# Kernel optimization log

Hardware: AMD Instinct MI355X
Metric: run time of the kernel (lower is better)

## Reference

```python
import jax, jax.numpy as jnp
import numpy as np

ALPHA = 0.2          # LeakyReLU negative slope
NEG_INF = -9e15      # masking value from the original module


def setup_inputs() -> dict:
    key = jax.random.key(0)
    kw, ka, k1, k2, k3 = jax.random.split(key, 5)
    B, N1, N2, F, O = 4, 2048, 2048, 256, 256
    word = jax.random.normal(kw, (B, N2, F), dtype=jnp.float32)
    # 0/1 hypergraph incidence matrix (float, as in the torch module)
    adj = jax.random.randint(ka, (B, N1, N2), 0, 2).astype(jnp.float32)
    stdv = 1.0 / np.sqrt(O)
    W1 = jax.random.uniform(k1, (F, O), jnp.float32, -stdv, stdv)
    W2 = jax.random.uniform(k2, (F, O), jnp.float32, -stdv, stdv)
    w3 = jax.random.uniform(k3, (2 * O, 1), jnp.float32, -stdv, stdv)
    return {"word": word, "adj": adj, "W1": W1, "W2": W2, "w3": w3}


def reference(word, adj, W1, W2, w3):
    # word: [B, N2, F]; adj: [B, N1, N2]; W1/W2: [F, O]; w3: [2O, 1]
    O = W1.shape[1]
    # mean-pool neighbor features per hyperedge (row-normalized adj)
    deg = jnp.sum(adj, axis=-1, keepdims=True)                 # [B, N1, 1]
    deg = jnp.where(deg > 0, deg, jnp.ones_like(deg))
    mp = jnp.matmul(adj / deg, word)                           # [B, N1, F]
    # The original builds 4D tensors h1[b,i,j,:] = adj[b,i,j]*word[b,j,:] and
    # h_mp[b,i,j,:] = adj[b,i,j]*mp[b,i,:], projects both and dots with w3.
    # Since scaling commutes with the linear maps, the scalar score is
    #   adj[b,i,j] * (word[b,j] @ W1 @ w3_a + mp[b,i] @ W2 @ w3_b)
    w3a = w3[:O, 0]                                            # pairs with w1h
    w3b = w3[O:, 0]                                            # pairs with w2h
    s1 = jnp.einsum('bnf,fo,o->bn', word, W1, w3a)             # [B, N2]
    s2 = jnp.einsum('bnf,fo,o->bn', mp, W2, w3b)               # [B, N1]
    pre = adj * (s2[:, :, None] + s1[:, None, :])              # [B, N1, N2]
    alpha = jnp.exp(jax.nn.leaky_relu(pre, ALPHA))
    attention = jnp.where(adj > 0, alpha, NEG_INF)
    attention_edge = jax.nn.softmax(attention, axis=2)         # over N2
    edge = jnp.matmul(attention_edge, word)                    # [B, N1, F]
    return edge
```

## Files before the change

kernel.cpp:

```cpp
#include <hip/hip_runtime.h>

#define B 4
#define N 2048
#define F 256
#define O 256
#define LOG2E 1.4426950408889634f
#define NEG_BIG -9000000000000000.0f

typedef _Float16 f16;
typedef f16 f16x8 __attribute__((ext_vector_type(8)));
typedef f16 f16x4 __attribute__((ext_vector_type(4)));
typedef float f32x16 __attribute__((ext_vector_type(16)));

#define WS_V1 0
#define WS_V2 256
#define WS_T1 512
#define WS_T2 (512 + B*N)
#define WS_S2 (512 + 2*B*N)
#define WS_CR (512 + 3*B*N)
#define WS_WN (512 + 4*B*N)
#define WT_OFF (1u << 20)
#define MK_OFF (6u << 20)

__device__ __forceinline__ float alpha_of(float pre2) {
  return __builtin_amdgcn_exp2f(fmaxf(pre2, 0.2f * pre2));
}

__global__ __launch_bounds__(256) void k_v(const float* __restrict__ W1,
                                           const float* __restrict__ W2,
                                           const float* __restrict__ w3,
                                           float* __restrict__ ws) {
  int tid = threadIdx.x;
  int lane = tid & 63;
  int f = blockIdx.x * 4 + (tid >> 6);
  float a = 0.f, b = 0.f;
  #pragma unroll
  for (int k = 0; k < 4; ++k) {
    int o = lane + 64 * k;
    a += W1[f * O + o] * w3[o];
    b += W2[f * O + o] * w3[O + o];
  }
  #pragma unroll
  for (int off = 32; off > 0; off >>= 1) {
    a += __shfl_down(a, off);
    b += __shfl_down(b, off);
  }
  if (lane == 0) {
    ws[WS_V1 + f] = a;
    ws[WS_V2 + f] = b;
  }
}

__global__ __launch_bounds__(256) void k_prep(const float* __restrict__ word,
                                              float* __restrict__ ws,
                                              f16* __restrict__ wordT) {
  __shared__ float v1s[F], v2s[F];
  __shared__ __align__(16) f16 tile[F][40];
  int t = threadIdx.x;
  int k0 = blockIdx.x * 32;
  int b = blockIdx.y;

  if (t < 64)       ((float4*)v1s)[t]      = ((const float4*)(ws + WS_V1))[t];
  else if (t < 128) ((float4*)v2s)[t - 64] = ((const float4*)(ws + WS_V2))[t - 64];
  __syncthreads();

  int r = t >> 3;
  int cg = t & 7;
  const float* wrow = word + ((size_t)(b * N + k0 + r)) * F;
  float a = 0.f, bb = 0.f;
  #pragma unroll
  for (int i = 0; i < 8; ++i) {
    int c = i * 32 + cg * 4;
    float4 w = *(const float4*)(wrow + c);
    float4 x1 = *(const float4*)(v1s + c);
    float4 x2 = *(const float4*)(v2s + c);
    a  += w.x * x1.x + w.y * x1.y + w.z * x1.z + w.w * x1.w;
    bb += w.x * x2.x + w.y * x2.y + w.z * x2.z + w.w * x2.w;
    tile[c + 0][r] = (f16)w.x;
    tile[c + 1][r] = (f16)w.y;
    tile[c + 2][r] = (f16)w.z;
    tile[c + 3][r] = (f16)w.w;
  }
  #pragma unroll
  for (int off = 4; off > 0; off >>= 1) {
    a  += __shfl_down(a, off);
    bb += __shfl_down(bb, off);
  }
  if (cg == 0) {
    ws[WS_T1 + b * N + k0 + r] = a * LOG2E;
    ws[WS_T2 + b * N + k0 + r] = bb;
  }
  __syncthreads();

  f16* dst = wordT + ((size_t)(b * F + t)) * N + k0;
  *(f16x8*)(dst + 0)  = *(const f16x8*)&tile[t][0];
  *(f16x8*)(dst + 8)  = *(const f16x8*)&tile[t][8];
  *(f16x8*)(dst + 16) = *(const f16x8*)&tile[t][16];
  *(f16x8*)(dst + 24) = *(const f16x8*)&tile[t][24];
}

__global__ __launch_bounds__(256) void k_stats(const float* __restrict__ adj,
                                               float* __restrict__ ws,
                                               unsigned char* __restrict__ mask) {
  int row = blockIdx.x;
  int b = row >> 11;
  int t = threadIdx.x;
  int wid = t >> 6, lane = t & 63;
  const float* arow = adj + (size_t)row * N;
  const float* t1b = ws + WS_T1 + b * N;
  const float* t2b = ws + WS_T2 + b * N;

  float4 a0 = *(const float4*)(arow + t * 8);
  float4 a1 = *(const float4*)(arow + t * 8 + 4);
  float4 u0 = *(const float4*)(t2b + t * 8);
  float4 u1 = *(const float4*)(t2b + t * 8 + 4);
  float deg = a0.x + a0.y + a0.z + a0.w + a1.x + a1.y + a1.z + a1.w;
  float dot = a0.x * u0.x + a0.y * u0.y + a0.z * u0.z + a0.w * u0.w +
              a1.x * u1.x + a1.y * u1.y + a1.z * u1.z + a1.w * u1.w;
  unsigned mb = (a0.x > 0.f ? 1u : 0u) | (a0.y > 0.f ? 2u : 0u) |
                (a0.z > 0.f ? 4u : 0u) | (a0.w > 0.f ? 8u : 0u) |
                (a1.x > 0.f ? 16u : 0u) | (a1.y > 0.f ? 32u : 0u) |
                (a1.z > 0.f ? 64u : 0u) | (a1.w > 0.f ? 128u : 0u);
  mask[(size_t)row * 256 + t] = (unsigned char)mb;

  #pragma unroll
  for (int off = 32; off > 0; off >>= 1) {
    deg += __shfl_down(deg, off);
    dot += __shfl_down(dot, off);
  }
  __shared__ float rd[4], rt[4], rm[4], rz[4];
  if (lane == 0) { rd[wid] = deg; rt[wid] = dot; }
  __syncthreads();
  deg = rd[0] + rd[1] + rd[2] + rd[3];
  dot = rt[0] + rt[1] + rt[2] + rt[3];
  float degc = deg > 0.f ? deg : 1.f;
  float s2p = (dot / degc) * LOG2E;

  float4 p0 = *(const float4*)(t1b + t * 8);
  float4 p1 = *(const float4*)(t1b + t * 8 + 4);
  float al[8];
  al[0] = (mb & 1)   ? alpha_of(p0.x + s2p) : NEG_BIG;
  al[1] = (mb & 2)   ? alpha_of(p0.y + s2p) : NEG_BIG;
  al[2] = (mb & 4)   ? alpha_of(p0.z + s2p) : NEG_BIG;
  al[3] = (mb & 8)   ? alpha_of(p0.w + s2p) : NEG_BIG;
  al[4] = (mb & 16)  ? alpha_of(p1.x + s2p) : NEG_BIG;
  al[5] = (mb & 32)  ? alpha_of(p1.y + s2p) : NEG_BIG;
  al[6] = (mb & 64)  ? alpha_of(p1.z + s2p) : NEG_BIG;
  al[7] = (mb & 128) ? alpha_of(p1.w + s2p) : NEG_BIG;
  float m = NEG_BIG;
  #pragma unroll
  for (int j = 0; j < 8; ++j) m = fmaxf(m, al[j]);
  #pragma unroll
  for (int off = 32; off > 0; off >>= 1) m = fmaxf(m, __shfl_down(m, off));
  if (lane == 0) rm[wid] = m;
  __syncthreads();
  m = fmaxf(fmaxf(rm[0], rm[1]), fmaxf(rm[2], rm[3]));

  float negmL = -m * LOG2E;
  float z = 0.f;
  #pragma unroll
  for (int j = 0; j < 8; ++j) z += __builtin_amdgcn_exp2f(fmaf(al[j], LOG2E, negmL));
  #pragma unroll
  for (int off = 32; off > 0; off >>= 1) z += __shfl_down(z, off);
  if (lane == 0) rz[wid] = z;
  __syncthreads();
  if (t == 0) {
    z = rz[0] + rz[1] + rz[2] + rz[3];
    ws[WS_S2 + row] = s2p;
    if (deg > 0.f) {
      ws[WS_CR + row] = negmL - log2f(z);
      ws[WS_WN + row] = 0.f;
    } else {
      ws[WS_CR + row] = 0.f;
      ws[WS_WN + row] = 1.0f / (float)N;
    }
  }
}

__global__ __launch_bounds__(512, 2) void k_gemm(const f16* __restrict__ wordT,
                                                 const unsigned char* __restrict__ maskg,
                                                 const float* __restrict__ ws,
                                                 float* __restrict__ out) {
  __shared__ __align__(16) f16 Aw[2][8][512];
  __shared__ __align__(16) float t1S[N];
  __shared__ __align__(16) unsigned maskS[32][64];
  __shared__ float sSC[96];

  const int t = threadIdx.x;
  const int row0 = blockIdx.x * 32;
  const int b = row0 >> 11;

  *(float4*)&t1S[t * 4] = *(const float4*)(ws + WS_T1 + b * N + t * 4);
  *(uint4*)&maskS[t >> 4][(t & 15) * 4] =
      *(const uint4*)(maskg + (size_t)(row0 + (t >> 4)) * 256 + (t & 15) * 16);
  if (t < 32) {
    sSC[t]      = ws[WS_S2 + row0 + t];
    sSC[32 + t] = ws[WS_CR + row0 + t];
    sSC[64 + t] = ws[WS_WN + row0 + t];
  }
  __syncthreads();

  const int gl = t & 63;
  const int gc = t >> 6;
  const int grow = gl & 31;
  const int gkb = gc * 16 + (gl >> 5) * 8;
  const float rs2 = sSC[grow], rcr = sSC[32 + grow], rwn = sSC[64 + grow];

  const int lw = t & 63;
  const int wv = t >> 6;
  const int fcol = wv * 32 + (lw & 31);
  const f16* bptr = wordT + ((size_t)(b * F + fcol)) * N + (lw >> 5) * 8;

  f32x16 acc = {0.f,0.f,0.f,0.f,0.f,0.f,0.f,0.f,0.f,0.f,0.f,0.f,0.f,0.f,0.f,0.f};

  #define GENW(IT, BUF)                                                        \
    {                                                                          \
      const int kg = (IT) * 128 + gkb;                                         \
      const unsigned mw = maskS[grow][kg >> 5] >> (kg & 31);                   \
      const float4 tv0 = *(const float4*)&t1S[kg];                             \
      const float4 tv1 = *(const float4*)&t1S[kg + 4];                         \
      const float tvv[8] = {tv0.x, tv0.y, tv0.z, tv0.w,                        \
                            tv1.x, tv1.y, tv1.z, tv1.w};                       \
      f16x8 h;                                                                 \
      _Pragma("unroll")                                                        \
      for (int j = 0; j < 8; ++j) {                                            \
        float p = tvv[j] + rs2;                                                \
        float al = __builtin_amdgcn_exp2f(fmaxf(p, 0.2f * p));                 \
        float wsel = __builtin_amdgcn_exp2f(fmaf(al, LOG2E, rcr));             \
        float w = ((mw >> j) & 1u) ? wsel : rwn;                               \
        h[j] = (f16)w;                                                         \
      }                                                                        \
      *(f16x8*)&Aw[BUF][gc][gl * 8] = h;                                       \
    }

  GENW(0, 0)
  __syncthreads();

  for (int it = 0; it < 16; ++it) {
    const int cur = it & 1;
    f16x8 bf[8];
    const f16* bp = bptr + it * 128;
    #pragma unroll
    for (int c = 0; c < 8; ++c) bf[c] = *(const f16x8*)(bp + c * 16);
    if (it < 15) GENW(it + 1, cur ^ 1)
    #pragma unroll
    for (int c = 0; c < 8; ++c) {
      const f16x8 af = *(const f16x8*)&Aw[cur][c][lw * 8];
      acc = __builtin_amdgcn_mfma_f32_32x32x16_f16(af, bf[c], acc, 0, 0, 0);
    }
    __syncthreads();
  }

  #pragma unroll
  for (int reg = 0; reg < 16; ++reg) {
    int lr = (reg & 3) + 8 * (reg >> 2) + 4 * (lw >> 5);
    out[(size_t)(row0 + lr) * F + fcol] = acc[reg];
  }
}

extern "C" void kernel_launch(void* const* d_in, const int* in_sizes, int n_in,
                              void* d_out, int out_size, void* d_ws, size_t ws_size,
                              hipStream_t stream) {
  const float* word = (const float*)d_in[0];
  const float* adj  = (const float*)d_in[1];
  const float* W1   = (const float*)d_in[2];
  const float* W2   = (const float*)d_in[3];
  const float* w3   = (const float*)d_in[4];
  float* out = (float*)d_out;
  float* ws  = (float*)d_ws;
  f16* wordT = (f16*)((char*)d_ws + WT_OFF);
  unsigned char* mask = (unsigned char*)d_ws + MK_OFF;

  k_v<<<64, 256, 0, stream>>>(W1, W2, w3, ws);
  k_prep<<<dim3(N / 32, B), 256, 0, stream>>>(word, ws, wordT);
  k_stats<<<B * N, 256, 0, stream>>>(adj, ws, mask);
  k_gemm<<<(B * N) / 32, 512, 0, stream>>>(wordT, mask, ws, out);
}
```

Before: 148.5 us.

## Retile attention GEMM to 64-row blocks split across feature halves with MFMA-swizzled wordT

```diff
diff --git a/kernel.cpp b/kernel.cpp
--- a/kernel.cpp
+++ b/kernel.cpp
@@ -9,7 +9,6 @@
 
 typedef _Float16 f16;
 typedef f16 f16x8 __attribute__((ext_vector_type(8)));
-typedef f16 f16x4 __attribute__((ext_vector_type(4)));
 typedef float f32x16 __attribute__((ext_vector_type(16)));
 
 #define WS_V1 0
@@ -92,11 +91,16 @@
   }
   __syncthreads();
 
-  f16* dst = wordT + ((size_t)(b * F + t)) * N + k0;
-  *(f16x8*)(dst + 0)  = *(const f16x8*)&tile[t][0];
-  *(f16x8*)(dst + 8)  = *(const f16x8*)&tile[t][8];
-  *(f16x8*)(dst + 16) = *(const f16x8*)&tile[t][16];
-  *(f16x8*)(dst + 24) = *(const f16x8*)&tile[t][24];
+  size_t base = (size_t)b * F * N;
+  #pragma unroll
+  for (int i = 0; i < 4; ++i) {
+    int idx = t + 256 * i;
+    int ft = idx >> 7, c = (idx >> 6) & 1, l = idx & 63;
+    int f = ft * 32 + (l & 31);
+    int rr = c * 16 + ((l >> 5) * 8);
+    f16x8 h = *(const f16x8*)&tile[f][rr];
+    *(f16x8*)(wordT + base + ((size_t)((ft * 128 + (k0 >> 4) + c) * 64 + l)) * 8) = h;
+  }
 }
 
 __global__ __launch_bounds__(256) void k_stats(const float* __restrict__ adj,
@@ -177,75 +181,92 @@
   }
 }
 
-__global__ __launch_bounds__(512, 2) void k_gemm(const f16* __restrict__ wordT,
+__global__ __launch_bounds__(512, 1) void k_gemm(const f16* __restrict__ wordT,
                                                  const unsigned char* __restrict__ maskg,
                                                  const float* __restrict__ ws,
                                                  float* __restrict__ out) {
-  __shared__ __align__(16) f16 Aw[2][8][512];
+  __shared__ __align__(16) f16 Aw[2][2][8][512];
   __shared__ __align__(16) float t1S[N];
-  __shared__ __align__(16) unsigned maskS[32][64];
-  __shared__ float sSC[96];
+  __shared__ float sSC[192];
 
   const int t = threadIdx.x;
-  const int row0 = blockIdx.x * 32;
+  const int rb = blockIdx.x >> 1, fh = blockIdx.x & 1;
+  const int row0 = rb * 64;
   const int b = row0 >> 11;
 
   *(float4*)&t1S[t * 4] = *(const float4*)(ws + WS_T1 + b * N + t * 4);
-  *(uint4*)&maskS[t >> 4][(t & 15) * 4] =
-      *(const uint4*)(maskg + (size_t)(row0 + (t >> 4)) * 256 + (t & 15) * 16);
-  if (t < 32) {
-    sSC[t]      = ws[WS_S2 + row0 + t];
-    sSC[32 + t] = ws[WS_CR + row0 + t];
-    sSC[64 + t] = ws[WS_WN + row0 + t];
+  if (t < 64) {
+    sSC[t]       = ws[WS_S2 + row0 + t];
+    sSC[64 + t]  = ws[WS_CR + row0 + t];
+    sSC[128 + t] = ws[WS_WN + row0 + t];
   }
   __syncthreads();
 
   const int gl = t & 63;
-  const int gc = t >> 6;
-  const int grow = gl & 31;
-  const int gkb = gc * 16 + (gl >> 5) * 8;
-  const float rs2 = sSC[grow], rcr = sSC[32 + grow], rwn = sSC[64 + grow];
+  const int gc = (t >> 6) & 3;
+  const int rh_g = t >> 8;
+  const int koff = (gl >> 5) * 8;
+  const int rowL = rh_g * 32 + (gl & 31);
+  const float rs2 = sSC[rowL], rcr = sSC[64 + rowL], rwn = sSC[128 + rowL];
+  const unsigned* mrow = (const unsigned*)(maskg + (size_t)(row0 + rowL) * 256);
 
   const int lw = t & 63;
   const int wv = t >> 6;
-  const int fcol = wv * 32 + (lw & 31);
-  const f16* bptr = wordT + ((size_t)(b * F + fcol)) * N + (lw >> 5) * 8;
+  const int rh = wv >> 2;
+  const int ftile = fh * 4 + (wv & 3);
+  const int fcol = ftile * 32 + (lw & 31);
+  const f16* wtb = wordT + (size_t)b * F * N;
 
   f32x16 acc = {0.f,0.f,0.f,0.f,0.f,0.f,0.f,0.f,0.f,0.f,0.f,0.f,0.f,0.f,0.f,0.f};
 
-  #define GENW(IT, BUF)                                                        \
+  #define GENW(IT, BUF, MW)                                                    \
     {                                                                          \
-      const int kg = (IT) * 128 + gkb;                                         \
-      const unsigned mw = maskS[grow][kg >> 5] >> (kg & 31);                   \
-      const float4 tv0 = *(const float4*)&t1S[kg];                             \
-      const float4 tv1 = *(const float4*)&t1S[kg + 4];                         \
-      const float tvv[8] = {tv0.x, tv0.y, tv0.z, tv0.w,                        \
-                            tv1.x, tv1.y, tv1.z, tv1.w};                       \
-      f16x8 h;                                                                 \
+      const int kb = (IT) * 128 + gc * 32 + koff;                              \
+      const float4 ta0 = *(const float4*)&t1S[kb];                             \
+      const float4 ta1 = *(const float4*)&t1S[kb + 4];                         \
+      const float4 tb0 = *(const float4*)&t1S[kb + 16];                        \
+      const float4 tb1 = *(const float4*)&t1S[kb + 20];                        \
+      const float ta[8] = {ta0.x, ta0.y, ta0.z, ta0.w, ta1.x, ta1.y, ta1.z, ta1.w}; \
+      const float tb[8] = {tb0.x, tb0.y, tb0.z, tb0.w, tb1.x, tb1.y, tb1.z, tb1.w}; \
+      const unsigned m0 = (MW) >> koff;                                        \
+      const unsigned m1 = (MW) >> (16 + koff);                                 \
+      f16x8 h0, h1;                                                            \
       _Pragma("unroll")                                                        \
       for (int j = 0; j < 8; ++j) {                                            \
-        float p = tvv[j] + rs2;                                                \
-        float al = __builtin_amdgcn_exp2f(fmaxf(p, 0.2f * p));                 \
-        float wsel = __builtin_amdgcn_exp2f(fmaf(al, LOG2E, rcr));             \
-        float w = ((mw >> j) & 1u) ? wsel : rwn;                               \
-        h[j] = (f16)w;                                                         \
+        float p0 = ta[j] + rs2;                                                \
+        float a0v = __builtin_amdgcn_exp2f(fmaxf(p0, 0.2f * p0));              \
+        float w0 = ((m0 >> j) & 1u) ? __builtin_amdgcn_exp2f(fmaf(a0v, LOG2E, rcr)) : rwn; \
+        h0[j] = (f16)w0;                                                       \
+        float p1 = tb[j] + rs2;                                                \
+        float a1v = __builtin_amdgcn_exp2f(fmaxf(p1, 0.2f * p1));              \
+        float w1 = ((m1 >> j) & 1u) ? __builtin_amdgcn_exp2f(fmaf(a1v, LOG2E, rcr)) : rwn; \
+        h1[j] = (f16)w1;                                                       \
       }                                                                        \
-      *(f16x8*)&Aw[BUF][gc][gl * 8] = h;                                       \
-    }
-
-  GENW(0, 0)
+      *(f16x8*)&Aw[BUF][rh_g][gc * 2][gl * 8]     = h0;                        \
+      *(f16x8*)&Aw[BUF][rh_g][gc * 2 + 1][gl * 8] = h1;                        \
+    }
+
+  {
+    unsigned mw0 = mrow[gc];
+    GENW(0, 0, mw0)
+  }
   __syncthreads();
 
   for (int it = 0; it < 16; ++it) {
     const int cur = it & 1;
+    const f16* bp = wtb + ((size_t)(ftile * 128 + it * 8) * 64 + lw) * 8;
     f16x8 bf[8];
-    const f16* bp = bptr + it * 128;
     #pragma unroll
-    for (int c = 0; c < 8; ++c) bf[c] = *(const f16x8*)(bp + c * 16);
-    if (it < 15) GENW(it + 1, cur ^ 1)
+    for (int c = 0; c < 8; ++c) bf[c] = *(const f16x8*)(bp + (size_t)c * 512);
+
+    if (it < 15) {
+      unsigned mwn = mrow[(it + 1) * 4 + gc];
+      GENW(it + 1, cur ^ 1, mwn)
+    }
+
     #pragma unroll
     for (int c = 0; c < 8; ++c) {
-      const f16x8 af = *(const f16x8*)&Aw[cur][c][lw * 8];
+      const f16x8 af = *(const f16x8*)&Aw[cur][rh][c][lw * 8];
       acc = __builtin_amdgcn_mfma_f32_32x32x16_f16(af, bf[c], acc, 0, 0, 0);
     }
     __syncthreads();
@@ -253,7 +274,7 @@
 
   #pragma unroll
   for (int reg = 0; reg < 16; ++reg) {
-    int lr = (reg & 3) + 8 * (reg >> 2) + 4 * (lw >> 5);
+    int lr = rh * 32 + (reg & 3) + 8 * (reg >> 2) + 4 * (lw >> 5);
     out[(size_t)(row0 + lr) * F + fcol] = acc[reg];
   }
 }
@@ -274,5 +295,5 @@
   k_v<<<64, 256, 0, stream>>>(W1, W2, w3, ws);
   k_prep<<<dim3(N / 32, B), 256, 0, stream>>>(word, ws, wordT);
   k_stats<<<B * N, 256, 0, stream>>>(adj, ws, mask);
-  k_gemm<<<(B * N) / 32, 512, 0, stream>>>(wordT, mask, ws, out);
-}
+  k_gemm<<<(B * N) / 64 * 2, 512, 0, stream>>>(wordT, mask, ws, out);
+}
```

Result: faster. 132.5 us (-10.8%).

## Materialize fp16 attention weights in stats kernel and swizzle word for direct-load GEMM

Applied to the files above, without the earlier changes.

```diff
diff --git a/kernel.cpp b/kernel.cpp
--- a/kernel.cpp
+++ b/kernel.cpp
@@ -9,18 +9,14 @@
 
 typedef _Float16 f16;
 typedef f16 f16x8 __attribute__((ext_vector_type(8)));
-typedef f16 f16x4 __attribute__((ext_vector_type(4)));
 typedef float f32x16 __attribute__((ext_vector_type(16)));
 
 #define WS_V1 0
 #define WS_V2 256
 #define WS_T1 512
 #define WS_T2 (512 + B*N)
-#define WS_S2 (512 + 2*B*N)
-#define WS_CR (512 + 3*B*N)
-#define WS_WN (512 + 4*B*N)
 #define WT_OFF (1u << 20)
-#define MK_OFF (6u << 20)
+#define W_OFF  (8u << 20)
 
 __device__ __forceinline__ float alpha_of(float pre2) {
   return __builtin_amdgcn_exp2f(fmaxf(pre2, 0.2f * pre2));
@@ -92,16 +88,21 @@
   }
   __syncthreads();
 
-  f16* dst = wordT + ((size_t)(b * F + t)) * N + k0;
-  *(f16x8*)(dst + 0)  = *(const f16x8*)&tile[t][0];
-  *(f16x8*)(dst + 8)  = *(const f16x8*)&tile[t][8];
-  *(f16x8*)(dst + 16) = *(const f16x8*)&tile[t][16];
-  *(f16x8*)(dst + 24) = *(const f16x8*)&tile[t][24];
+  size_t base = (size_t)b * F * N;
+  #pragma unroll
+  for (int i = 0; i < 4; ++i) {
+    int idx = t + 256 * i;
+    int ft = idx >> 7, c = (idx >> 6) & 1, l = idx & 63;
+    int f = ft * 32 + (l & 31);
+    int rr = c * 16 + ((l >> 5) * 8);
+    f16x8 h = *(const f16x8*)&tile[f][rr];
+    *(f16x8*)(wordT + base + ((size_t)((ft * 128 + (k0 >> 4) + c) * 64 + l)) * 8) = h;
+  }
 }
 
 __global__ __launch_bounds__(256) void k_stats(const float* __restrict__ adj,
                                                float* __restrict__ ws,
-                                               unsigned char* __restrict__ mask) {
+                                               f16* __restrict__ Wm) {
   int row = blockIdx.x;
   int b = row >> 11;
   int t = threadIdx.x;
@@ -121,7 +122,6 @@
                 (a0.z > 0.f ? 4u : 0u) | (a0.w > 0.f ? 8u : 0u) |
                 (a1.x > 0.f ? 16u : 0u) | (a1.y > 0.f ? 32u : 0u) |
                 (a1.z > 0.f ? 64u : 0u) | (a1.w > 0.f ? 128u : 0u);
-  mask[(size_t)row * 256 + t] = (unsigned char)mb;
 
   #pragma unroll
   for (int off = 32; off > 0; off >>= 1) {
@@ -164,97 +164,58 @@
   for (int off = 32; off > 0; off >>= 1) z += __shfl_down(z, off);
   if (lane == 0) rz[wid] = z;
   __syncthreads();
-  if (t == 0) {
-    z = rz[0] + rz[1] + rz[2] + rz[3];
-    ws[WS_S2 + row] = s2p;
-    if (deg > 0.f) {
-      ws[WS_CR + row] = negmL - log2f(z);
-      ws[WS_WN + row] = 0.f;
-    } else {
-      ws[WS_CR + row] = 0.f;
-      ws[WS_WN + row] = 1.0f / (float)N;
-    }
-  }
-}
-
-__global__ __launch_bounds__(512, 2) void k_gemm(const f16* __restrict__ wordT,
-                                                 const unsigned char* __restrict__ maskg,
-                                                 const float* __restrict__ ws,
-                                                 float* __restrict__ out) {
-  __shared__ __align__(16) f16 Aw[2][8][512];
-  __shared__ __align__(16) float t1S[N];
-  __shared__ __align__(16) unsigned maskS[32][64];
-  __shared__ float sSC[96];
-
+  float zf = rz[0] + rz[1] + rz[2] + rz[3];
+
+  float cr, wn;
+  if (deg > 0.f) { cr = negmL - log2f(zf); wn = 0.f; }
+  else           { cr = 0.f;               wn = 1.0f / (float)N; }
+  f16x8 hw;
+  #pragma unroll
+  for (int j = 0; j < 8; ++j) {
+    float w = ((mb >> j) & 1u) ? __builtin_amdgcn_exp2f(fmaf(al[j], LOG2E, cr)) : wn;
+    hw[j] = (f16)w;
+  }
+  *(f16x8*)(Wm + (size_t)row * N + t * 8) = hw;
+}
+
+__global__ __launch_bounds__(128) void k_gemm(const f16* __restrict__ Wm,
+                                              const f16* __restrict__ wordT,
+                                              float* __restrict__ out) {
   const int t = threadIdx.x;
-  const int row0 = blockIdx.x * 32;
-  const int b = row0 >> 11;
-
-  *(float4*)&t1S[t * 4] = *(const float4*)(ws + WS_T1 + b * N + t * 4);
-  *(uint4*)&maskS[t >> 4][(t & 15) * 4] =
-      *(const uint4*)(maskg + (size_t)(row0 + (t >> 4)) * 256 + (t & 15) * 16);
-  if (t < 32) {
-    sSC[t]      = ws[WS_S2 + row0 + t];
-    sSC[32 + t] = ws[WS_CR + row0 + t];
-    sSC[64 + t] = ws[WS_WN + row0 + t];
-  }
-  __syncthreads();
-
-  const int gl = t & 63;
-  const int gc = t >> 6;
-  const int grow = gl & 31;
-  const int gkb = gc * 16 + (gl >> 5) * 8;
-  const float rs2 = sSC[grow], rcr = sSC[32 + grow], rwn = sSC[64 + grow];
-
-  const int lw = t & 63;
-  const int wv = t >> 6;
-  const int fcol = wv * 32 + (lw & 31);
-  const f16* bptr = wordT + ((size_t)(b * F + fcol)) * N + (lw >> 5) * 8;
-
-  f32x16 acc = {0.f,0.f,0.f,0.f,0.f,0.f,0.f,0.f,0.f,0.f,0.f,0.f,0.f,0.f,0.f,0.f};
-
-  #define GENW(IT, BUF)                                                        \
-    {                                                                          \
-      const int kg = (IT) * 128 + gkb;                                         \
-      const unsigned mw = maskS[grow][kg >> 5] >> (kg & 31);                   \
-      const float4 tv0 = *(const float4*)&t1S[kg];                             \
-      const float4 tv1 = *(const float4*)&t1S[kg + 4];                         \
-      const float tvv[8] = {tv0.x, tv0.y, tv0.z, tv0.w,                        \
-                            tv1.x, tv1.y, tv1.z, tv1.w};                       \
-      f16x8 h;                                                                 \
-      _Pragma("unroll")                                                        \
-      for (int j = 0; j < 8; ++j) {                                            \
-        float p = tvv[j] + rs2;                                                \
-        float al = __builtin_amdgcn_exp2f(fmaxf(p, 0.2f * p));                 \
-        float wsel = __builtin_amdgcn_exp2f(fmaf(al, LOG2E, rcr));             \
-        float w = ((mw >> j) & 1u) ? wsel : rwn;                               \
-        h[j] = (f16)w;                                                         \
-      }                                                                        \
-      *(f16x8*)&Aw[BUF][gc][gl * 8] = h;                                       \
-    }
-
-  GENW(0, 0)
-  __syncthreads();
-
-  for (int it = 0; it < 16; ++it) {
-    const int cur = it & 1;
-    f16x8 bf[8];
-    const f16* bp = bptr + it * 128;
-    #pragma unroll
-    for (int c = 0; c < 8; ++c) bf[c] = *(const f16x8*)(bp + c * 16);
-    if (it < 15) GENW(it + 1, cur ^ 1)
+  const int l = t & 63;
+  const int w = t >> 6;
+  const int fg = blockIdx.x & 3;
+  const int mp = blockIdx.x >> 2;
+  const int m0 = (mp * 2 + w) * 32;
+  const int b = m0 >> 11;
+  const int f0 = fg * 64;
+
+  const f16* Ap = Wm + (size_t)(m0 + (l & 31)) * N + (l >> 5) * 8;
+  const f16* Bp = wordT + (size_t)b * F * N + ((size_t)(fg * 2) * 128 * 64 + l) * 8;
+
+  f32x16 acc0 = {0.f,0.f,0.f,0.f,0.f,0.f,0.f,0.f,0.f,0.f,0.f,0.f,0.f,0.f,0.f,0.f};
+  f32x16 acc1 = {0.f,0.f,0.f,0.f,0.f,0.f,0.f,0.f,0.f,0.f,0.f,0.f,0.f,0.f,0.f,0.f};
+
+  for (int kc = 0; kc < 128; kc += 8) {
+    f16x8 a[8], p[8], q[8];
     #pragma unroll
     for (int c = 0; c < 8; ++c) {
-      const f16x8 af = *(const f16x8*)&Aw[cur][c][lw * 8];
-      acc = __builtin_amdgcn_mfma_f32_32x32x16_f16(af, bf[c], acc, 0, 0, 0);
+      a[c] = *(const f16x8*)(Ap + (size_t)(kc + c) * 16);
+      p[c] = *(const f16x8*)(Bp + (size_t)(kc + c) * 512);
+      q[c] = *(const f16x8*)(Bp + 65536 + (size_t)(kc + c) * 512);
     }
-    __syncthreads();
+    #pragma unroll
+    for (int c = 0; c < 8; ++c) {
+      acc0 = __builtin_amdgcn_mfma_f32_32x32x16_f16(a[c], p[c], acc0, 0, 0, 0);
+      acc1 = __builtin_amdgcn_mfma_f32_32x32x16_f16(a[c], q[c], acc1, 0, 0, 0);
+    }
   }
 
   #pragma unroll
   for (int reg = 0; reg < 16; ++reg) {
-    int lr = (reg & 3) + 8 * (reg >> 2) + 4 * (lw >> 5);
-    out[(size_t)(row0 + lr) * F + fcol] = acc[reg];
+    int row = m0 + (reg & 3) + 8 * (reg >> 2) + 4 * (l >> 5);
+    out[(size_t)row * F + f0 + (l & 31)]      = acc0[reg];
+    out[(size_t)row * F + f0 + 32 + (l & 31)] = acc1[reg];
   }
 }
 
@@ -269,10 +230,10 @@
   float* out = (float*)d_out;
   float* ws  = (float*)d_ws;
   f16* wordT = (f16*)((char*)d_ws + WT_OFF);
-  unsigned char* mask = (unsigned char*)d_ws + MK_OFF;
+  f16* Wm    = (f16*)((char*)d_ws + W_OFF);
 
   k_v<<<64, 256, 0, stream>>>(W1, W2, w3, ws);
   k_prep<<<dim3(N / 32, B), 256, 0, stream>>>(word, ws, wordT);
-  k_stats<<<B * N, 256, 0, stream>>>(adj, ws, mask);
-  k_gemm<<<(B * N) / 32, 512, 0, stream>>>(wordT, mask, ws, out);
-}
+  k_stats<<<B * N, 256, 0, stream>>>(adj, ws, Wm);
+  k_gemm<<<512, 128, 0, stream>>>(Wm, wordT, out);
+}
```

Measured after the change: 169.6 us. +14.2%, slower.
